# Optimization experiments

Hardware: AMD Instinct MI355X
Metric: run time of the kernel (lower is better)

Reference implementation:

```python
import jax, jax.numpy as jnp
import numpy as np

N = 100_000   # nodes
E = 3_200_000 # edges
K = 3         # num_stacks
T = 4         # num_layers (shared weights)
H = 16        # hidden channels of conv1
EPS = 1e-5    # BatchNorm eps


def setup_inputs() -> dict:
    key = jax.random.key(0)
    ks = jax.random.split(key, 12)
    def glorot(k, shape):
        fan = shape[-2] + shape[-1]
        return jax.random.normal(k, shape, jnp.float32) * (2.0 / fan) ** 0.5
    return {
        "x": jax.random.normal(ks[0], (N, 1), jnp.float32),
        "edge_index": jax.random.randint(ks[1], (2, E), 0, N, jnp.int32),
        "edge_weight": jax.random.uniform(ks[2], (E,), jnp.float32),
        # conv1: in=1, out=16  (init_weight [K,Fin,Fout], shared weight [K,Fout,Fout], root [K,Fin,Fout], bias [K,Fout])
        "conv1_init_w": glorot(ks[3], (K, 1, H)),
        "conv1_w": glorot(ks[4], (K, H, H)),
        "conv1_root_w": glorot(ks[5], (K, 1, H)),
        "conv1_bias": jnp.zeros((K, H), jnp.float32),
        # BatchNorm1d(16) in eval mode: running stats + affine params
        "bn1_gamma": jnp.ones((H,), jnp.float32),
        "bn1_beta": jnp.zeros((H,), jnp.float32),
        "bn1_mean": jnp.zeros((H,), jnp.float32),
        "bn1_var": jnp.ones((H,), jnp.float32),
        # conv2: in=16, out=1, act=None
        "conv2_init_w": glorot(ks[6], (K, H, 1)),
        "conv2_w": glorot(ks[7], (K, 1, 1)),
        "conv2_root_w": glorot(ks[8], (K, H, 1)),
        "conv2_bias": jnp.zeros((K, 1), jnp.float32),
    }


def _gcn_norm(edge_index, edge_weight):
    # ARMAConv uses gcn_norm with add_self_loops=False
    row, col = edge_index[0], edge_index[1]
    deg = jax.ops.segment_sum(edge_weight, col, num_segments=N)
    dis = jnp.where(deg > 0, jax.lax.rsqrt(jnp.maximum(deg, 1e-12)), 0.0)
    norm = dis[row] * edge_weight * dis[col]
    return row, col, norm


def _arma(x, row, col, norm, init_w, w, root_w, bias, act):
    # x: [N, Fin]; out per stack: [K, N, Fout]
    root = jnp.einsum('nf,kfo->kno', x, root_w) + bias[:, None, :]
    out = jnp.einsum('nf,kfo->kno', x, init_w)
    for t in range(T):
        if t > 0:
            out = jnp.einsum('kno,kop->knp', out, w)  # shared weight
        msg = out[:, row, :] * norm[None, :, None]     # [K, E, F] gather + scale
        out = jax.ops.segment_sum(msg.transpose(1, 0, 2), col, num_segments=N)  # [N, K, F]
        out = out.transpose(1, 0, 2) + root            # scatter-add + skip (root)
        if act:
            out = jax.nn.relu(out)
    return out.mean(axis=0)  # mean over stacks -> [N, Fout]


def reference(x, edge_index, edge_weight,
              conv1_init_w, conv1_w, conv1_root_w, conv1_bias,
              bn1_gamma, bn1_beta, bn1_mean, bn1_var,
              conv2_init_w, conv2_w, conv2_root_w, conv2_bias):
    row, col, norm = _gcn_norm(edge_index, edge_weight)
    h = _arma(x, row, col, norm, conv1_init_w, conv1_w, conv1_root_w, conv1_bias, act=True)
    # BatchNorm1d (eval) + ReLU; dropout is identity in eval
    h = (h - bn1_mean) * jax.lax.rsqrt(bn1_var + EPS) * bn1_gamma + bn1_beta
    h = jax.nn.relu(h)
    h = _arma(h, row, col, norm, conv2_init_w, conv2_w, conv2_root_w, conv2_bias, act=False)
    return jax.nn.sigmoid(h)  # [N, 1]
```

## Files before the change

### kernel.cpp

```cpp
#include <hip/hip_runtime.h>
#include <math.h>

#define NN 100000
#define NE 3200000
#define NB 782
#define BCAP 4608
#define EPB 2048
#define BN_EPS 1e-5f

static inline size_t alignup(size_t v) { return (v + 255) & ~size_t(255); }

__device__ inline unsigned short f2bf(float x) {
  unsigned u = __float_as_uint(x);
  u += 0x7FFF + ((u >> 16) & 1);
  return (unsigned short)(u >> 16);
}
__device__ inline float bf2f(unsigned short h) {
  return __uint_as_float((unsigned)h << 16);
}

__global__ void k_bin(const int* __restrict__ row, const int* __restrict__ col,
                      const float* __restrict__ ew, int* __restrict__ gfill,
                      int2* __restrict__ bin) {
  __shared__ int cnt[NB];
  __shared__ int base[NB];
  for (int i = threadIdx.x; i < NB; i += 256) cnt[i] = 0;
  __syncthreads();
  int e0 = blockIdx.x * EPB;
  int nE = min(EPB, NE - e0);
  for (int i = threadIdx.x; i < nE; i += 256) atomicAdd(&cnt[col[e0 + i] >> 7], 1);
  __syncthreads();
  for (int i = threadIdx.x; i < NB; i += 256) {
    int c = cnt[i];
    base[i] = (c > 0) ? atomicAdd(&gfill[i], c) : 0;
    cnt[i] = 0;
  }
  __syncthreads();
  for (int i = threadIdx.x; i < nE; i += 256) {
    int e = e0 + i;
    int c = col[e], b = c >> 7;
    int pos = base[b] + atomicAdd(&cnt[b], 1);
    if (pos < BCAP)
      bin[(size_t)b * BCAP + pos] =
          make_int2(row[e] | ((c & 127) << 17), __float_as_int(ew[e]));
  }
}

__global__ void k_build(const int* __restrict__ gfill, const int2* __restrict__ bin,
                        int* __restrict__ csr, float* __restrict__ dis,
                        int* __restrict__ nstart, int* __restrict__ ncnt) {
  __shared__ int cnt[128];
  __shared__ float degw[128];
  __shared__ int off[129];
  int b = blockIdx.x;
  int nb = min(gfill[b], BCAP);
  const int2* gb = bin + (size_t)b * BCAP;
  for (int i = threadIdx.x; i < 128; i += 256) { cnt[i] = 0; degw[i] = 0.f; }
  __syncthreads();
  for (int i = threadIdx.x; i < nb; i += 256) {
    int2 v = gb[i];
    int c = (v.x >> 17) & 127;
    atomicAdd(&cnt[c], 1);
    atomicAdd(&degw[c], __int_as_float(v.y));
  }
  __syncthreads();
  if (threadIdx.x == 0) {
    int s = 0;
    for (int c = 0; c < 128; ++c) { off[c] = s; s += cnt[c]; }
    off[128] = s;
  }
  __syncthreads();
  int gbase = b * BCAP;
  for (int c = threadIdx.x; c < 128; c += 256) {
    int n = b * 128 + c;
    if (n < NN) {
      nstart[n] = gbase + off[c];
      ncnt[n] = cnt[c];
      float d = degw[c];
      dis[n] = (d > 0.f) ? rsqrtf(fmaxf(d, 1e-12f)) : 0.f;
    }
  }
  __syncthreads();
  for (int i = threadIdx.x; i < 128; i += 256) cnt[i] = 0;
  __syncthreads();
  int* cb = csr + (size_t)b * BCAP;
  for (int i = threadIdx.x; i < nb; i += 256) {
    int2 v = gb[i];
    int c = (v.x >> 17) & 127;
    int pos = off[c] + atomicAdd(&cnt[c], 1);
    float w = __int_as_float(v.y);
    int q = (int)fminf(fmaf(w, 32767.f, 0.5f), 32767.f);
    cb[pos] = (v.x & 0x1FFFF) | (q << 17);
  }
}

__global__ void k_init1(const float* __restrict__ x, const float* __restrict__ rw,
                        const float* __restrict__ bias, const float* __restrict__ dis,
                        float* __restrict__ root1, float* __restrict__ s) {
  int idx = blockIdx.x * 256 + threadIdx.x;
  if (idx >= NN * 16) return;
  int n = idx >> 4, f = idx & 15;
  float xv = x[n];
  if (f == 0) s[n] = dis[n] * xv;
  root1[n * 48 + f]      = xv * rw[f]      + bias[f];
  root1[n * 48 + 16 + f] = xv * rw[16 + f] + bias[16 + f];
  root1[n * 48 + 32 + f] = xv * rw[32 + f] + bias[32 + f];
}

__global__ void k_prop_first(const float* __restrict__ s, const float* __restrict__ root,
                             ushort4* __restrict__ outp, const int* __restrict__ csr,
                             const int* __restrict__ nstart, const int* __restrict__ ncnt,
                             const float* __restrict__ dis, const float* __restrict__ w,
                             const float* __restrict__ iw) {
  __shared__ float ws[768];
  for (int i = threadIdx.x; i < 768; i += 256) ws[i] = w[i];
  __syncthreads();
  int f = threadIdx.x & 15;
  int n = (blockIdx.x * 256 + threadIdx.x) >> 4;
  if (n >= NN) return;
  int e0 = nstart[n], cnt = ncnt[n];
  float g = 0.f;
  for (int i = f; i < cnt; i += 16) {
    int e = csr[e0 + i];
    float we = (float)((unsigned)e >> 17) * (1.f / 32767.f);
    g = fmaf(we, s[e & 0x1FFFF], g);
  }
  #pragma unroll
  for (int d = 8; d; d >>= 1) g += __shfl_xor(g, d, 16);
  float dn = dis[n];
  float dg = dn * g;
  float a0 = fmaxf(fmaf(dg, iw[f],      root[n * 48 + f]),      0.f);
  float a1 = fmaxf(fmaf(dg, iw[16 + f], root[n * 48 + 16 + f]), 0.f);
  float a2 = fmaxf(fmaf(dg, iw[32 + f], root[n * 48 + 32 + f]), 0.f);
  float n0 = 0.f, n1 = 0.f, n2 = 0.f;
  #pragma unroll
  for (int f2 = 0; f2 < 16; ++f2) {
    float b0 = __shfl(a0, f2, 16);
    float b1 = __shfl(a1, f2, 16);
    float b2v = __shfl(a2, f2, 16);
    n0 = fmaf(b0, ws[f2 * 16 + f], n0);
    n1 = fmaf(b1, ws[256 + f2 * 16 + f], n1);
    n2 = fmaf(b2v, ws[512 + f2 * 16 + f], n2);
  }
  ushort4 pk;
  pk.x = f2bf(dn * n0); pk.y = f2bf(dn * n1); pk.z = f2bf(dn * n2); pk.w = 0;
  outp[(size_t)n * 16 + f] = pk;
}

template <bool APPLY_W>
__global__ void k_prop16(const ushort4* __restrict__ in, const float* __restrict__ root,
                         ushort4* __restrict__ outp, const int* __restrict__ csr,
                         const int* __restrict__ nstart, const int* __restrict__ ncnt,
                         const float* __restrict__ dis, const float* __restrict__ w,
                         const float* __restrict__ bng, const float* __restrict__ bnb,
                         const float* __restrict__ bnm, const float* __restrict__ bnv,
                         const float* __restrict__ iw2, const float* __restrict__ rw2,
                         const float* __restrict__ b2,
                         float4* __restrict__ root2, float4* __restrict__ o2) {
  __shared__ float ws[768];
  if (APPLY_W) {
    for (int i = threadIdx.x; i < 768; i += 256) ws[i] = w[i];
    __syncthreads();
  }
  int f = threadIdx.x & 15;
  int n = (blockIdx.x * 256 + threadIdx.x) >> 4;
  if (n >= NN) return;
  int e0 = nstart[n], cnt = ncnt[n];
  float a0 = 0.f, a1 = 0.f, a2 = 0.f;
  int i = 0;
  for (; i + 8 <= cnt; i += 8) {
    int e[8];
    ushort4 v[8];
    #pragma unroll
    for (int j = 0; j < 8; ++j) e[j] = csr[e0 + i + j];
    #pragma unroll
    for (int j = 0; j < 8; ++j) v[j] = in[(size_t)(e[j] & 0x1FFFF) * 16 + f];
    #pragma unroll
    for (int j = 0; j < 8; ++j) {
      float we = (float)((unsigned)e[j] >> 17) * (1.f / 32767.f);
      a0 = fmaf(we, bf2f(v[j].x), a0);
      a1 = fmaf(we, bf2f(v[j].y), a1);
      a2 = fmaf(we, bf2f(v[j].z), a2);
    }
  }
  for (; i + 4 <= cnt; i += 4) {
    int e[4];
    ushort4 v[4];
    #pragma unroll
    for (int j = 0; j < 4; ++j) e[j] = csr[e0 + i + j];
    #pragma unroll
    for (int j = 0; j < 4; ++j) v[j] = in[(size_t)(e[j] & 0x1FFFF) * 16 + f];
    #pragma unroll
    for (int j = 0; j < 4; ++j) {
      float we = (float)((unsigned)e[j] >> 17) * (1.f / 32767.f);
      a0 = fmaf(we, bf2f(v[j].x), a0);
      a1 = fmaf(we, bf2f(v[j].y), a1);
      a2 = fmaf(we, bf2f(v[j].z), a2);
    }
  }
  for (; i < cnt; ++i) {
    int e = csr[e0 + i];
    float we = (float)((unsigned)e >> 17) * (1.f / 32767.f);
    ushort4 v = in[(size_t)(e & 0x1FFFF) * 16 + f];
    a0 = fmaf(we, bf2f(v.x), a0);
    a1 = fmaf(we, bf2f(v.y), a1);
    a2 = fmaf(we, bf2f(v.z), a2);
  }
  float dn = dis[n];
  a0 = fmaxf(fmaf(dn, a0, root[n * 48 + f]), 0.f);
  a1 = fmaxf(fmaf(dn, a1, root[n * 48 + 16 + f]), 0.f);
  a2 = fmaxf(fmaf(dn, a2, root[n * 48 + 32 + f]), 0.f);
  if (APPLY_W) {
    float n0 = 0.f, n1 = 0.f, n2 = 0.f;
    #pragma unroll
    for (int f2 = 0; f2 < 16; ++f2) {
      float b0 = __shfl(a0, f2, 16);
      float b1 = __shfl(a1, f2, 16);
      float b2v = __shfl(a2, f2, 16);
      n0 = fmaf(b0, ws[f2 * 16 + f], n0);
      n1 = fmaf(b1, ws[256 + f2 * 16 + f], n1);
      n2 = fmaf(b2v, ws[512 + f2 * 16 + f], n2);
    }
    ushort4 pk;
    pk.x = f2bf(dn * n0); pk.y = f2bf(dn * n1); pk.z = f2bf(dn * n2); pk.w = 0;
    outp[(size_t)n * 16 + f] = pk;
  } else {
    float mean = (a0 + a1 + a2) * (1.f / 3.f);
    float hv = fmaxf((mean - bnm[f]) * rsqrtf(bnv[f] + BN_EPS) * bng[f] + bnb[f], 0.f);
    float d0 = hv * iw2[f],      r0 = hv * rw2[f];
    float d1 = hv * iw2[16 + f], r1 = hv * rw2[16 + f];
    float d2 = hv * iw2[32 + f], r2 = hv * rw2[32 + f];
    #pragma unroll
    for (int d = 8; d; d >>= 1) {
      d0 += __shfl_xor(d0, d, 16); r0 += __shfl_xor(r0, d, 16);
      d1 += __shfl_xor(d1, d, 16); r1 += __shfl_xor(r1, d, 16);
      d2 += __shfl_xor(d2, d, 16); r2 += __shfl_xor(r2, d, 16);
    }
    if (f == 0) {
      float4 rt, oo;
      rt.x = r0 + b2[0]; rt.y = r1 + b2[1]; rt.z = r2 + b2[2]; rt.w = 0.f;
      oo.x = dn * d0; oo.y = dn * d1; oo.z = dn * d2; oo.w = 0.f;
      root2[n] = rt;
      o2[n] = oo;
    }
  }
}

template <bool LAST>
__global__ void k_prop1(const float4* __restrict__ in, const float4* __restrict__ root,
                        float4* __restrict__ outp, float* __restrict__ outf,
                        const int* __restrict__ csr,
                        const int* __restrict__ nstart, const int* __restrict__ ncnt,
                        const float* __restrict__ dis, const float* __restrict__ w2) {
  int lane = threadIdx.x & 15;
  int n = (blockIdx.x * 256 + threadIdx.x) >> 4;
  if (n >= NN) return;
  int e0 = nstart[n], cnt = ncnt[n];
  float a0 = 0.f, a1 = 0.f, a2 = 0.f;
  for (int i = lane; i < cnt; i += 16) {
    int e = csr[e0 + i];
    float we = (float)((unsigned)e >> 17) * (1.f / 32767.f);
    float4 src = in[e & 0x1FFFF];
    a0 = fmaf(we, src.x, a0);
    a1 = fmaf(we, src.y, a1);
    a2 = fmaf(we, src.z, a2);
  }
  #pragma unroll
  for (int d = 8; d; d >>= 1) {
    a0 += __shfl_xor(a0, d, 16);
    a1 += __shfl_xor(a1, d, 16);
    a2 += __shfl_xor(a2, d, 16);
  }
  if (lane == 0) {
    float dn = dis[n];
    float4 rt = root[n];
    if (LAST) {
      float s = fmaf(dn, a0, rt.x) + fmaf(dn, a1, rt.y) + fmaf(dn, a2, rt.z);
      s *= (1.f / 3.f);
      outf[n] = 1.f / (1.f + expf(-s));
    } else {
      float4 oo;
      oo.x = dn * fmaf(dn, a0, rt.x) * w2[0];
      oo.y = dn * fmaf(dn, a1, rt.y) * w2[1];
      oo.z = dn * fmaf(dn, a2, rt.z) * w2[2];
      oo.w = 0.f;
      outp[n] = oo;
    }
  }
}

extern "C" void kernel_launch(void* const* d_in, const int* in_sizes, int n_in,
                              void* d_out, int out_size, void* d_ws, size_t ws_size,
                              hipStream_t stream) {
  const float* x     = (const float*)d_in[0];
  const int*   ei    = (const int*)d_in[1];
  const float* ew    = (const float*)d_in[2];
  const float* c1_iw = (const float*)d_in[3];
  const float* c1_w  = (const float*)d_in[4];
  const float* c1_rw = (const float*)d_in[5];
  const float* c1_b  = (const float*)d_in[6];
  const float* bn_g  = (const float*)d_in[7];
  const float* bn_b  = (const float*)d_in[8];
  const float* bn_m  = (const float*)d_in[9];
  const float* bn_v  = (const float*)d_in[10];
  const float* c2_iw = (const float*)d_in[11];
  const float* c2_w  = (const float*)d_in[12];
  const float* c2_rw = (const float*)d_in[13];
  const float* c2_b  = (const float*)d_in[14];
  float* out = (float*)d_out;

  char* p = (char*)d_ws;
  auto take = [&](size_t bytes) -> char* { char* r = p; p += alignup(bytes); return r; };
  int*     gfill = (int*)take((size_t)NB * 4);
  int2*    bin   = (int2*)take((size_t)NB * BCAP * 8);
  int*     csr   = (int*)take((size_t)NB * BCAP * 4);
  float*   dis   = (float*)take((size_t)NN * 4);
  int*     nst   = (int*)take((size_t)NN * 4);
  int*     ncn   = (int*)take((size_t)NN * 4);
  float*   root1 = (float*)take((size_t)NN * 48 * 4);
  float*   sbuf  = (float*)take((size_t)NN * 4);
  ushort4* bufA  = (ushort4*)take((size_t)NN * 16 * 8);
  ushort4* bufB  = (ushort4*)take((size_t)NN * 16 * 8);
  float4*  root2 = (float4*)take((size_t)NN * 16);
  float4*  o2A   = (float4*)take((size_t)NN * 16);
  float4*  o2B   = (float4*)take((size_t)NN * 16);

  hipMemsetAsync(gfill, 0, (size_t)NB * 4, stream);

  const int* row = ei;
  const int* col = ei + NE;

  const int gBin = (NE + EPB - 1) / EPB;
  const int gP   = (NN * 16 + 255) / 256;

  k_bin<<<gBin, 256, 0, stream>>>(row, col, ew, gfill, bin);
  k_build<<<NB, 256, 0, stream>>>(gfill, bin, csr, dis, nst, ncn);

  k_init1<<<gP, 256, 0, stream>>>(x, c1_rw, c1_b, dis, root1, sbuf);
  k_prop_first<<<gP, 256, 0, stream>>>(sbuf, root1, bufA, csr, nst, ncn, dis, c1_w, c1_iw);
  k_prop16<true ><<<gP, 256, 0, stream>>>(bufA, root1, bufB, csr, nst, ncn, dis, c1_w,
      nullptr, nullptr, nullptr, nullptr, nullptr, nullptr, nullptr, nullptr, nullptr);
  k_prop16<true ><<<gP, 256, 0, stream>>>(bufB, root1, bufA, csr, nst, ncn, dis, c1_w,
      nullptr, nullptr, nullptr, nullptr, nullptr, nullptr, nullptr, nullptr, nullptr);
  k_prop16<false><<<gP, 256, 0, stream>>>(bufA, root1, nullptr, csr, nst, ncn, dis, nullptr,
      bn_g, bn_b, bn_m, bn_v, c2_iw, c2_rw, c2_b, root2, o2A);

  k_prop1<false><<<gP, 256, 0, stream>>>(o2A, root2, o2B, nullptr, csr, nst, ncn, dis, c2_w);
  k_prop1<false><<<gP, 256, 0, stream>>>(o2B, root2, o2A, nullptr, csr, nst, ncn, dis, c2_w);
  k_prop1<false><<<gP, 256, 0, stream>>>(o2A, root2, o2B, nullptr, csr, nst, ncn, dis, c2_w);
  k_prop1<true ><<<gP, 256, 0, stream>>>(o2B, root2, nullptr, out, csr, nst, ncn, dis, c2_w);
}
```

Before: 416.1 us.

## Replace atomic fixed-capacity binning with histogram-scan-scatter compact CSR build

The one-pass bin kernel used global atomics into fixed-capacity buckets, and it silently dropped edges once a bucket overflowed. It is replaced by a per-block histogram, a column-wise exclusive scan, a bucket-total scan and a deterministic scatter into a compact edge array. This removes global atomic contention and the padded BCAP layout, and makes the bucketing exact. In exchange it adds three extra kernel launches, a second full read of col, and transposed strided reads of the count matrix in the scan.

```diff
diff --git a/kernel.cpp b/kernel.cpp
--- a/kernel.cpp
+++ b/kernel.cpp
@@ -4,8 +4,8 @@
 #define NN 100000
 #define NE 3200000
 #define NB 782
-#define BCAP 4608
-#define EPB 2048
+#define EPB 4096
+#define NBLK 782
 #define BN_EPS 1e-5f
 
 static inline size_t alignup(size_t v) { return (v + 255) & ~size_t(255); }
@@ -19,42 +19,115 @@
   return __uint_as_float((unsigned)h << 16);
 }
 
-__global__ void k_bin(const int* __restrict__ row, const int* __restrict__ col,
-                      const float* __restrict__ ew, int* __restrict__ gfill,
-                      int2* __restrict__ bin) {
+__global__ void k_hist(const int* __restrict__ col, int* __restrict__ cntm) {
   __shared__ int cnt[NB];
-  __shared__ int base[NB];
   for (int i = threadIdx.x; i < NB; i += 256) cnt[i] = 0;
   __syncthreads();
   int e0 = blockIdx.x * EPB;
   int nE = min(EPB, NE - e0);
   for (int i = threadIdx.x; i < nE; i += 256) atomicAdd(&cnt[col[e0 + i] >> 7], 1);
   __syncthreads();
-  for (int i = threadIdx.x; i < NB; i += 256) {
-    int c = cnt[i];
-    base[i] = (c > 0) ? atomicAdd(&gfill[i], c) : 0;
+  int* dst = cntm + (size_t)blockIdx.x * NB;
+  for (int i = threadIdx.x; i < NB; i += 256) dst[i] = cnt[i];
+}
+
+__global__ void k_scanb(const int* __restrict__ cntm, int* __restrict__ basemT,
+                        int* __restrict__ btot) {
+  __shared__ int s[NBLK];
+  __shared__ int c[256];
+  const int NCH = (NBLK + 3) / 4;
+  int q = blockIdx.x, t = threadIdx.x;
+  for (int i = t; i < NBLK; i += 256) s[i] = cntm[(size_t)i * NB + q];
+  __syncthreads();
+  if (t < NCH) {
+    int b0 = 4 * t, sum = 0;
+    #pragma unroll
+    for (int j = 0; j < 4; ++j) if (b0 + j < NBLK) sum += s[b0 + j];
+    c[t] = sum;
+  }
+  __syncthreads();
+  for (int d = 1; d < NCH; d <<= 1) {
+    int v = (t < NCH && t >= d) ? c[t - d] : 0;
+    __syncthreads();
+    if (t < NCH) c[t] += v;
+    __syncthreads();
+  }
+  if (t < NCH) {
+    int b0 = 4 * t;
+    int run = (t > 0) ? c[t - 1] : 0;
+    #pragma unroll
+    for (int j = 0; j < 4; ++j)
+      if (b0 + j < NBLK) { int v = s[b0 + j]; s[b0 + j] = run; run += v; }
+  }
+  __syncthreads();
+  int* dst = basemT + (size_t)q * NBLK;
+  for (int i = t; i < NBLK; i += 256) dst[i] = s[i];
+  if (t == 0) btot[q] = c[NCH - 1];
+}
+
+__global__ void k_scanq(const int* __restrict__ btot, int* __restrict__ gbase) {
+  __shared__ int s[NB];
+  __shared__ int c[256];
+  const int NCH = (NB + 3) / 4;
+  int t = threadIdx.x;
+  for (int i = t; i < NB; i += 256) s[i] = btot[i];
+  __syncthreads();
+  if (t < NCH) {
+    int b0 = 4 * t, sum = 0;
+    #pragma unroll
+    for (int j = 0; j < 4; ++j) if (b0 + j < NB) sum += s[b0 + j];
+    c[t] = sum;
+  }
+  __syncthreads();
+  for (int d = 1; d < NCH; d <<= 1) {
+    int v = (t < NCH && t >= d) ? c[t - d] : 0;
+    __syncthreads();
+    if (t < NCH) c[t] += v;
+    __syncthreads();
+  }
+  if (t < NCH) {
+    int b0 = 4 * t;
+    int run = (t > 0) ? c[t - 1] : 0;
+    #pragma unroll
+    for (int j = 0; j < 4; ++j)
+      if (b0 + j < NB) { int v = s[b0 + j]; s[b0 + j] = run; run += v; }
+  }
+  __syncthreads();
+  for (int i = t; i < NB; i += 256) gbase[i] = s[i];
+}
+
+__global__ void k_scat(const int* __restrict__ row, const int* __restrict__ col,
+                       const float* __restrict__ ew, const int* __restrict__ basemT,
+                       const int* __restrict__ gbase, int2* __restrict__ bin) {
+  __shared__ int baseL[NB];
+  __shared__ int cnt[NB];
+  int b = blockIdx.x, t = threadIdx.x;
+  for (int i = t; i < NB; i += 256) {
+    baseL[i] = gbase[i] + basemT[(size_t)i * NBLK + b];
     cnt[i] = 0;
   }
   __syncthreads();
-  for (int i = threadIdx.x; i < nE; i += 256) {
+  int e0 = b * EPB;
+  int nE = min(EPB, NE - e0);
+  for (int i = t; i < nE; i += 256) {
     int e = e0 + i;
-    int c = col[e], b = c >> 7;
-    int pos = base[b] + atomicAdd(&cnt[b], 1);
-    if (pos < BCAP)
-      bin[(size_t)b * BCAP + pos] =
-          make_int2(row[e] | ((c & 127) << 17), __float_as_int(ew[e]));
-  }
-}
-
-__global__ void k_build(const int* __restrict__ gfill, const int2* __restrict__ bin,
+    int cc = col[e], q = cc >> 7;
+    int r = atomicAdd(&cnt[q], 1);
+    bin[baseL[q] + r] = make_int2(row[e] | ((cc & 127) << 17), __float_as_int(ew[e]));
+  }
+}
+
+__global__ void k_build(const int* __restrict__ gbase, const int* __restrict__ btot,
+                        const int2* __restrict__ bin,
                         int* __restrict__ csr, float* __restrict__ dis,
                         int* __restrict__ nstart, int* __restrict__ ncnt) {
   __shared__ int cnt[128];
   __shared__ float degw[128];
   __shared__ int off[129];
   int b = blockIdx.x;
-  int nb = min(gfill[b], BCAP);
-  const int2* gb = bin + (size_t)b * BCAP;
+  int gb0 = gbase[b];
+  int nb = btot[b];
+  const int2* gb = bin + gb0;
   for (int i = threadIdx.x; i < 128; i += 256) { cnt[i] = 0; degw[i] = 0.f; }
   __syncthreads();
   for (int i = threadIdx.x; i < nb; i += 256) {
@@ -70,11 +143,10 @@
     off[128] = s;
   }
   __syncthreads();
-  int gbase = b * BCAP;
   for (int c = threadIdx.x; c < 128; c += 256) {
     int n = b * 128 + c;
     if (n < NN) {
-      nstart[n] = gbase + off[c];
+      nstart[n] = gb0 + off[c];
       ncnt[n] = cnt[c];
       float d = degw[c];
       dis[n] = (d > 0.f) ? rsqrtf(fmaxf(d, 1e-12f)) : 0.f;
@@ -83,7 +155,7 @@
   __syncthreads();
   for (int i = threadIdx.x; i < 128; i += 256) cnt[i] = 0;
   __syncthreads();
-  int* cb = csr + (size_t)b * BCAP;
+  int* cb = csr + gb0;
   for (int i = threadIdx.x; i < nb; i += 256) {
     int2 v = gb[i];
     int c = (v.x >> 17) & 127;
@@ -311,30 +383,33 @@
 
   char* p = (char*)d_ws;
   auto take = [&](size_t bytes) -> char* { char* r = p; p += alignup(bytes); return r; };
-  int*     gfill = (int*)take((size_t)NB * 4);
-  int2*    bin   = (int2*)take((size_t)NB * BCAP * 8);
-  int*     csr   = (int*)take((size_t)NB * BCAP * 4);
-  float*   dis   = (float*)take((size_t)NN * 4);
-  int*     nst   = (int*)take((size_t)NN * 4);
-  int*     ncn   = (int*)take((size_t)NN * 4);
-  float*   root1 = (float*)take((size_t)NN * 48 * 4);
-  float*   sbuf  = (float*)take((size_t)NN * 4);
-  ushort4* bufA  = (ushort4*)take((size_t)NN * 16 * 8);
-  ushort4* bufB  = (ushort4*)take((size_t)NN * 16 * 8);
-  float4*  root2 = (float4*)take((size_t)NN * 16);
-  float4*  o2A   = (float4*)take((size_t)NN * 16);
-  float4*  o2B   = (float4*)take((size_t)NN * 16);
-
-  hipMemsetAsync(gfill, 0, (size_t)NB * 4, stream);
+  int*     cntm   = (int*)take((size_t)NBLK * NB * 4);
+  int*     basemT = (int*)take((size_t)NB * NBLK * 4);
+  int*     btot   = (int*)take((size_t)NB * 4);
+  int*     gbase  = (int*)take((size_t)NB * 4);
+  int2*    bin    = (int2*)take((size_t)NE * 8);
+  int*     csr    = (int*)take((size_t)NE * 4);
+  float*   dis    = (float*)take((size_t)NN * 4);
+  int*     nst    = (int*)take((size_t)NN * 4);
+  int*     ncn    = (int*)take((size_t)NN * 4);
+  float*   root1  = (float*)take((size_t)NN * 48 * 4);
+  float*   sbuf   = (float*)take((size_t)NN * 4);
+  ushort4* bufA   = (ushort4*)take((size_t)NN * 16 * 8);
+  ushort4* bufB   = (ushort4*)take((size_t)NN * 16 * 8);
+  float4*  root2  = (float4*)take((size_t)NN * 16);
+  float4*  o2A    = (float4*)take((size_t)NN * 16);
+  float4*  o2B    = (float4*)take((size_t)NN * 16);
 
   const int* row = ei;
   const int* col = ei + NE;
 
-  const int gBin = (NE + EPB - 1) / EPB;
-  const int gP   = (NN * 16 + 255) / 256;
-
-  k_bin<<<gBin, 256, 0, stream>>>(row, col, ew, gfill, bin);
-  k_build<<<NB, 256, 0, stream>>>(gfill, bin, csr, dis, nst, ncn);
+  const int gP = (NN * 16 + 255) / 256;
+
+  k_hist <<<NBLK, 256, 0, stream>>>(col, cntm);
+  k_scanb<<<NB, 256, 0, stream>>>(cntm, basemT, btot);
+  k_scanq<<<1, 256, 0, stream>>>(btot, gbase);
+  k_scat <<<NBLK, 256, 0, stream>>>(row, col, ew, basemT, gbase, bin);
+  k_build<<<NB, 256, 0, stream>>>(gbase, btot, bin, csr, dis, nst, ncn);
 
   k_init1<<<gP, 256, 0, stream>>>(x, c1_rw, c1_b, dis, root1, sbuf);
   k_prop_first<<<gP, 256, 0, stream>>>(sbuf, root1, bufA, csr, nst, ncn, dis, c1_w, c1_iw);
```

After: 386.6 us. -7.1%, faster.
